# Optimization experiments

Measured on AMD Instinct MI355X. Metric: run time of the kernel, lower is better.

Reference implementation:

```python
import jax, jax.numpy as jnp
import numpy as np

N = 40000      # nodes
E = 320000     # edges (avg degree 8)
F_IN = 128     # input channels
H = 4          # attention heads
C = 64         # per-head hidden channels (hidden_features_size entries)
HC = H * C     # 256, width after head concat
OUT = 64       # output classes
BN_EPS = 1e-5
NEG_SLOPE = 0.2


def setup_inputs() -> dict:
    key = jax.random.key(0)
    ks = jax.random.split(key, 16)
    s1 = 1.0 / np.sqrt(F_IN)
    s2 = 1.0 / np.sqrt(HC)
    return {
        "x": jax.random.normal(ks[0], (N, F_IN), jnp.float32),
        "edge_index": jax.random.randint(ks[1], (2, E), 0, N, dtype=jnp.int64),
        "W1": jax.random.normal(ks[2], (F_IN, HC), jnp.float32) * s1,
        "a1_src": jax.random.normal(ks[3], (H, C), jnp.float32) * s2,
        "a1_dst": jax.random.normal(ks[4], (H, C), jnp.float32) * s2,
        "b1": jnp.zeros((HC,), jnp.float32),
        # BatchNorm1d(256)
        "bn1_gamma": jnp.ones((HC,), jnp.float32),
        "bn1_beta": jnp.zeros((HC,), jnp.float32),
        "W2": jax.random.normal(ks[5], (HC, HC), jnp.float32) * s2,
        "a2_src": jax.random.normal(ks[6], (H, C), jnp.float32) * s2,
        "a2_dst": jax.random.normal(ks[7], (H, C), jnp.float32) * s2,
        "b2": jnp.zeros((HC,), jnp.float32),
        # final projection Linear(256 -> 64)
        "linW": jax.random.normal(ks[8], (HC, OUT), jnp.float32) * s2,
        "linb": jnp.zeros((OUT,), jnp.float32),
    }


def gat_conv(x, W, a_src, a_dst, bias, src, dst):
    """PyG GATConv (concat=True, add_self_loops=False, negative_slope=0.2)."""
    h = (x @ W).reshape(-1, H, C)                       # [N,H,C]
    e_src = jnp.einsum("nhc,hc->nh", h, a_src)          # [N,H]
    e_dst = jnp.einsum("nhc,hc->nh", h, a_dst)          # [N,H]
    # per-edge unnormalized attention, message src -> dst
    e = jax.nn.leaky_relu(e_src[src] + e_dst[dst], NEG_SLOPE)   # [E,H]
    # segment softmax over incoming edges of each dst node
    m = jax.ops.segment_max(e, dst, num_segments=N)             # [N,H]
    p = jnp.exp(e - jax.lax.stop_gradient(m)[dst])              # [E,H]
    denom = jax.ops.segment_sum(p, dst, num_segments=N)         # [N,H]
    alpha = p / (denom[dst] + 1e-16)                            # [E,H]
    # weighted scatter-sum aggregation
    out = jax.ops.segment_sum(h[src] * alpha[:, :, None], dst, num_segments=N)  # [N,H,C]
    return out.reshape(-1, HC) + bias


def batch_norm(x, gamma, beta):
    mean = jnp.mean(x, axis=0)
    var = jnp.mean(jnp.square(x - mean), axis=0)
    return (x - mean) * jax.lax.rsqrt(var + BN_EPS) * gamma + beta


def reference(x, edge_index, W1, a1_src, a1_dst, b1, bn1_gamma, bn1_beta,
              W2, a2_src, a2_dst, b2, linW, linb):
    src, dst = edge_index[0], edge_index[1]
    h1 = gat_conv(x, W1, a1_src, a1_dst, b1, src, dst)
    h1 = jax.nn.elu(batch_norm(h1, bn1_gamma, bn1_beta))
    # dropout is identity in eval mode
    h2 = gat_conv(h1, W2, a2_src, a2_dst, b2, src, dst)
    # JumpingKnowledge 'max': elementwise max over layer outputs
    jk = jnp.maximum(h1, h2)
    return jk @ linW + linb
```

## Files before the change

kernel.cpp:

```cpp
#include <hip/hip_runtime.h>
#include <math.h>

#define N_NODES 40000
#define N_EDGES 320000
#define F_IN 128
#define NHEAD 4
#define HC 256
#define NOUT 64
#define SLOTCAP 40
#define BN_RBLK 40

typedef __attribute__((ext_vector_type(8))) __bf16 bf16x8;
typedef __attribute__((ext_vector_type(4))) float f32x4;

static __device__ __forceinline__ unsigned short f2bf(float f) {
    union { float f; unsigned u; } v; v.f = f;
    unsigned r = v.u + 0x7FFFu + ((v.u >> 16) & 1u);
    return (unsigned short)(r >> 16);
}
static __device__ __forceinline__ float bf2f(unsigned short s) {
    union { unsigned u; float f; } v; v.u = ((unsigned)s) << 16;
    return v.f;
}

__global__ __launch_bounds__(256) void prep_kernel(const float* __restrict__ W1,
                                                   const float* __restrict__ W2,
                                                   const float* __restrict__ linW,
                                                   unsigned short* __restrict__ W1t,
                                                   unsigned short* __restrict__ W2t,
                                                   unsigned short* __restrict__ linWt,
                                                   int* __restrict__ zero_ints,
                                                   float* __restrict__ bnacc) {
    int b = blockIdx.x, tid = threadIdx.x;
    if (b < 128) {
        int t = b * 256 + tid;
        int k = t >> 8, n = t & 255;
        W1t[n * 128 + k] = f2bf(W1[t]);
    } else if (b < 384) {
        int t = (b - 128) * 256 + tid;
        int k = t >> 8, n = t & 255;
        W2t[n * 256 + k] = f2bf(W2[t]);
    } else if (b < 448) {
        int t = (b - 384) * 256 + tid;
        int k = t >> 6, n = t & 63;
        linWt[n * 256 + k] = f2bf(linW[t]);
    } else if (b < 488) {
        int i = (b - 448) * 1024 + tid * 4;
        if (i < 40004) *(int4*)(zero_ints + i) = make_int4(0, 0, 0, 0);
    } else {
        if (tid < 512) bnacc[tid] = 0.f;
    }
}

template <int AMODE, int SCATTER>
__global__ __launch_bounds__(256) void gemm_wide(const void* __restrict__ Aptr,
                                                 const unsigned short* __restrict__ Bt,
                                                 const float* __restrict__ sc,
                                                 unsigned short* __restrict__ Cb,
                                                 const float* __restrict__ asrc,
                                                 const float* __restrict__ adst,
                                                 float* __restrict__ es,
                                                 float* __restrict__ ed,
                                                 int K,
                                                 const int* __restrict__ ei,
                                                 int* __restrict__ cursor,
                                                 unsigned short* __restrict__ esorted) {
    __shared__ unsigned short As[2][64 * 32];
    __shared__ unsigned short Bs[2][256 * 32];
    int tid = threadIdx.x;
    if (SCATTER && blockIdx.x >= N_NODES / 64) {
        int e = (blockIdx.x - N_NODES / 64) * 256 + tid;
        if (e < N_EDGES) {
            int d = ei[N_EDGES + e];
            int s = ei[e];
            int pos = atomicAdd(&cursor[d], 1);
            esorted[d * SLOTCAP + pos] = (unsigned short)s;
        }
        return;
    }
    int row0 = blockIdx.x * 64;
    int w = tid >> 6, lane = tid & 63;
    int quad = lane >> 4, l16 = lane & 15;
    f32x4 acc[4][4];
#pragma unroll
    for (int mi = 0; mi < 4; ++mi)
#pragma unroll
        for (int ni = 0; ni < 4; ++ni) acc[mi][ni] = (f32x4){0.f, 0.f, 0.f, 0.f};

    int srow = tid >> 2, schunk = (tid & 3) * 8;
    int brow = tid >> 1, bchunk = (tid & 1) * 16;

    float4 pa0, pa1;
    int4 pai;
    int4 pb[4];
    if (AMODE == 1) {
        const float* Af = (const float*)Aptr;
        size_t base = (size_t)(row0 + srow) * K + schunk;
        pa0 = *(const float4*)(Af + base);
        pa1 = *(const float4*)(Af + base + 4);
    } else {
        pai = *(const int4*)((const unsigned short*)Aptr + (size_t)(row0 + srow) * K + schunk);
    }
    {
        const unsigned short* s0 = Bt + (size_t)brow * K + bchunk;
        const unsigned short* s1 = Bt + (size_t)(128 + brow) * K + bchunk;
        pb[0] = *(const int4*)s0; pb[1] = *(const int4*)(s0 + 8);
        pb[2] = *(const int4*)s1; pb[3] = *(const int4*)(s1 + 8);
    }

    for (int kc = 0; kc < K; kc += 32) {
        int buf = (kc >> 5) & 1;
        union { int4 v; unsigned short u[8]; } aS;
        if (AMODE == 1) {
            aS.u[0] = f2bf(pa0.x); aS.u[1] = f2bf(pa0.y);
            aS.u[2] = f2bf(pa0.z); aS.u[3] = f2bf(pa0.w);
            aS.u[4] = f2bf(pa1.x); aS.u[5] = f2bf(pa1.y);
            aS.u[6] = f2bf(pa1.z); aS.u[7] = f2bf(pa1.w);
        } else {
            union { int4 v; unsigned short u[8]; } a;
            a.v = pai;
#pragma unroll
            for (int j = 0; j < 8; ++j) {
                int c = kc + schunk + j;
                float v = bf2f(a.u[j]) * sc[c] + sc[HC + c];
                v = v > 0.f ? v : (__expf(v) - 1.f);
                aS.u[j] = f2bf(v);
            }
        }
        int4 bS0 = pb[0], bS1 = pb[1], bS2 = pb[2], bS3 = pb[3];
        int kn = kc + 32;
        if (kn < K) {
            if (AMODE == 1) {
                const float* Af = (const float*)Aptr;
                size_t base = (size_t)(row0 + srow) * K + kn + schunk;
                pa0 = *(const float4*)(Af + base);
                pa1 = *(const float4*)(Af + base + 4);
            } else {
                pai = *(const int4*)((const unsigned short*)Aptr +
                                     (size_t)(row0 + srow) * K + kn + schunk);
            }
            const unsigned short* s0 = Bt + (size_t)brow * K + kn + bchunk;
            const unsigned short* s1 = Bt + (size_t)(128 + brow) * K + kn + bchunk;
            pb[0] = *(const int4*)s0; pb[1] = *(const int4*)(s0 + 8);
            pb[2] = *(const int4*)s1; pb[3] = *(const int4*)(s1 + 8);
        }
        *(int4*)(&As[buf][srow * 32 + schunk]) = aS.v;
        *(int4*)(&Bs[buf][brow * 32 + bchunk]) = bS0;
        *(int4*)(&Bs[buf][brow * 32 + bchunk + 8]) = bS1;
        *(int4*)(&Bs[buf][(128 + brow) * 32 + bchunk]) = bS2;
        *(int4*)(&Bs[buf][(128 + brow) * 32 + bchunk + 8]) = bS3;
        __syncthreads();
        bf16x8 af[4], bfr[4];
#pragma unroll
        for (int mi = 0; mi < 4; ++mi)
            af[mi] = *(const bf16x8*)(&As[buf][(mi * 16 + l16) * 32 + quad * 8]);
#pragma unroll
        for (int ni = 0; ni < 4; ++ni)
            bfr[ni] = *(const bf16x8*)(&Bs[buf][(w * 64 + ni * 16 + l16) * 32 + quad * 8]);
#pragma unroll
        for (int mi = 0; mi < 4; ++mi)
#pragma unroll
            for (int ni = 0; ni < 4; ++ni)
                acc[mi][ni] = __builtin_amdgcn_mfma_f32_16x16x32_bf16(
                    af[mi], bfr[ni], acc[mi][ni], 0, 0, 0);
    }
#pragma unroll
    for (int mi = 0; mi < 4; ++mi)
#pragma unroll
        for (int ni = 0; ni < 4; ++ni) {
            int r0 = row0 + mi * 16 + quad * 4;
            int c = w * 64 + ni * 16 + l16;
#pragma unroll
            for (int r = 0; r < 4; ++r)
                Cb[(size_t)(r0 + r) * HC + c] = f2bf(acc[mi][ni][r]);
        }
    float as_v[4], ad_v[4];
#pragma unroll
    for (int ni = 0; ni < 4; ++ni) {
        int cl = ni * 16 + l16;
        as_v[ni] = asrc[w * 64 + cl];
        ad_v[ni] = adst[w * 64 + cl];
    }
#pragma unroll
    for (int mi = 0; mi < 4; ++mi)
#pragma unroll
        for (int r = 0; r < 4; ++r) {
            float s = 0.f, d = 0.f;
#pragma unroll
            for (int ni = 0; ni < 4; ++ni) {
                s += acc[mi][ni][r] * as_v[ni];
                d += acc[mi][ni][r] * ad_v[ni];
            }
#pragma unroll
            for (int off = 1; off < 16; off <<= 1) {
                s += __shfl_xor(s, off);
                d += __shfl_xor(d, off);
            }
            if (l16 == 0) {
                int row = row0 + mi * 16 + quad * 4 + r;
                es[(size_t)row * NHEAD + w] = s;
                ed[(size_t)row * NHEAD + w] = d;
            }
        }
}

__global__ __launch_bounds__(256) void aggregate_kernel(const unsigned short* __restrict__ h,
                                                        const float* __restrict__ es,
                                                        const float* __restrict__ ed,
                                                        const int* __restrict__ deg,
                                                        const unsigned short* __restrict__ esorted,
                                                        const float* __restrict__ bias,
                                                        unsigned short* __restrict__ outb,
                                                        float* __restrict__ partials) {
    __shared__ float sdata[8][256];
    int tid = threadIdx.x;
    int wave = tid >> 6, lane = tid & 63;
    int half = lane >> 5, l = lane & 31;
    int nloc = wave * 2 + half;
    int node = blockIdx.x * 8 + nloc;
    int hh = l >> 3;
    float edv = ed[node * NHEAD + hh];
    int d = deg[node];
    int beg = node * SLOTCAP;
    float dsum = 0.f;
    float a[8] = {0.f, 0.f, 0.f, 0.f, 0.f, 0.f, 0.f, 0.f};
    for (int i = 0; i < d; i += 16) {
        int s[16];
        int4 hv[16];
        float ep[16];
#pragma unroll
        for (int j = 0; j < 16; ++j) {
            int slot = i + j;
            s[j] = esorted[beg + (slot < d ? slot : d - 1)];
        }
#pragma unroll
        for (int j = 0; j < 16; ++j)
            hv[j] = *(const int4*)(h + (size_t)s[j] * HC + l * 8);
#pragma unroll
        for (int j = 0; j < 16; ++j)
            ep[j] = es[s[j] * NHEAD + hh];
#pragma unroll
        for (int j = 0; j < 16; ++j) {
            float e = ep[j] + edv;
            e = e > 0.f ? e : 0.2f * e;
            float w = __expf(e);
            w = (i + j < d) ? w : 0.f;
            dsum += w;
            union { int4 v; unsigned short u[8]; } hu;
            hu.v = hv[j];
#pragma unroll
            for (int k = 0; k < 8; ++k) a[k] += w * bf2f(hu.u[k]);
        }
    }
    float inv = 1.f / (dsum + 1e-16f);
    float4 bv0 = *(const float4*)(bias + l * 8);
    float4 bv1 = *(const float4*)(bias + l * 8 + 4);
    float bb[8] = {bv0.x, bv0.y, bv0.z, bv0.w, bv1.x, bv1.y, bv1.z, bv1.w};
    float ov[8];
    union { int4 v; unsigned short u[8]; } o;
#pragma unroll
    for (int k = 0; k < 8; ++k) {
        ov[k] = a[k] * inv + bb[k];
        o.u[k] = f2bf(ov[k]);
    }
    *(int4*)(outb + (size_t)node * HC + l * 8) = o.v;
#pragma unroll
    for (int k = 0; k < 8; ++k) sdata[nloc][l * 8 + k] = ov[k];
    __syncthreads();
    {
        int c = tid;
        float s = 0.f, s2 = 0.f;
#pragma unroll
        for (int n = 0; n < 8; ++n) {
            float v = sdata[n][c];
            s += v; s2 += v * v;
        }
        float* pb = partials + (size_t)blockIdx.x * 512;
        pb[c] = s;
        pb[256 + c] = s2;
    }
}

__global__ __launch_bounds__(512) void aggregate2_fused(const unsigned short* __restrict__ h,
                                                        const float* __restrict__ es,
                                                        const float* __restrict__ ed,
                                                        const int* __restrict__ deg,
                                                        const unsigned short* __restrict__ esorted,
                                                        const float* __restrict__ bias,
                                                        const unsigned short* __restrict__ h1agg,
                                                        const float* __restrict__ bnsc,
                                                        const unsigned short* __restrict__ linWt,
                                                        const float* __restrict__ linb,
                                                        float* __restrict__ out) {
    __shared__ unsigned short jkS[16 * 264];
    __shared__ unsigned short BsF[64 * 264];
    int tid = threadIdx.x;
    {
        int n = tid >> 3, k0 = (tid & 7) * 32;
        const int4* src = (const int4*)(linWt + n * 256 + k0);
        int4 v0 = src[0], v1 = src[1], v2 = src[2], v3 = src[3];
        int4* dstp = (int4*)(&BsF[n * 264 + k0]);
        dstp[0] = v0; dstp[1] = v1; dstp[2] = v2; dstp[3] = v3;
    }
    int wave = tid >> 6, lane = tid & 63;
    int half = lane >> 5, l = lane & 31;
    int nloc = wave * 2 + half;
    int node = blockIdx.x * 16 + nloc;
    int hh = l >> 3;
    float edv = ed[node * NHEAD + hh];
    int d = deg[node];
    int beg = node * SLOTCAP;
    float dsum = 0.f;
    float a[8] = {0.f, 0.f, 0.f, 0.f, 0.f, 0.f, 0.f, 0.f};
    for (int i = 0; i < d; i += 8) {
        int s[8];
        int4 hv[8];
        float ep[8];
#pragma unroll
        for (int j = 0; j < 8; ++j) {
            int slot = i + j;
            s[j] = esorted[beg + (slot < d ? slot : d - 1)];
        }
#pragma unroll
        for (int j = 0; j < 8; ++j)
            hv[j] = *(const int4*)(h + (size_t)s[j] * HC + l * 8);
#pragma unroll
        for (int j = 0; j < 8; ++j)
            ep[j] = es[s[j] * NHEAD + hh];
#pragma unroll
        for (int j = 0; j < 8; ++j) {
            float e = ep[j] + edv;
            e = e > 0.f ? e : 0.2f * e;
            float w = __expf(e);
            w = (i + j < d) ? w : 0.f;
            dsum += w;
            union { int4 v; unsigned short u[8]; } hu;
            hu.v = hv[j];
#pragma unroll
            for (int k = 0; k < 8; ++k) a[k] += w * bf2f(hu.u[k]);
        }
    }
    float inv = 1.f / (dsum + 1e-16f);
    float4 bv0 = *(const float4*)(bias + l * 8);
    float4 bv1 = *(const float4*)(bias + l * 8 + 4);
    float bb[8] = {bv0.x, bv0.y, bv0.z, bv0.w, bv1.x, bv1.y, bv1.z, bv1.w};
    union { int4 v; unsigned short u[8]; } o;
    {
        union { int4 v; unsigned short u[8]; } h1u;
        h1u.v = *(const int4*)(h1agg + (size_t)node * HC + l * 8);
        float4 s0 = *(const float4*)(bnsc + l * 8);
        float4 s1 = *(const float4*)(bnsc + l * 8 + 4);
        float4 t0 = *(const float4*)(bnsc + HC + l * 8);
        float4 t1 = *(const float4*)(bnsc + HC + l * 8 + 4);
        float scv[8] = {s0.x, s0.y, s0.z, s0.w, s1.x, s1.y, s1.z, s1.w};
        float shv[8] = {t0.x, t0.y, t0.z, t0.w, t1.x, t1.y, t1.z, t1.w};
#pragma unroll
        for (int k = 0; k < 8; ++k) {
            float v = bf2f(h1u.u[k]) * scv[k] + shv[k];
            v = v > 0.f ? v : (__expf(v) - 1.f);
            o.u[k] = f2bf(fmaxf(v, a[k] * inv + bb[k]));
        }
    }
    *(int4*)(&jkS[nloc * 264 + l * 8]) = o.v;
    __syncthreads();
    if (wave < 4) {
        int quad = lane >> 4, l16 = lane & 15;
        f32x4 acc = (f32x4){0.f, 0.f, 0.f, 0.f};
#pragma unroll
        for (int kc = 0; kc < HC; kc += 32) {
            bf16x8 af = *(const bf16x8*)(&jkS[l16 * 264 + kc + quad * 8]);
            bf16x8 bfr = *(const bf16x8*)(&BsF[(wave * 16 + l16) * 264 + kc + quad * 8]);
            acc = __builtin_amdgcn_mfma_f32_16x16x32_bf16(af, bfr, acc, 0, 0, 0);
        }
        int row0 = blockIdx.x * 16 + quad * 4;
        int c = wave * 16 + l16;
        float bc = linb[c];
#pragma unroll
        for (int r = 0; r < 4; ++r)
            out[(size_t)(row0 + r) * NOUT + c] = acc[r] + bc;
    }
}

__global__ __launch_bounds__(256) void bn_reduce_kernel(const float* __restrict__ partials,
                                                        float* __restrict__ acc,
                                                        const float* __restrict__ gamma,
                                                        const float* __restrict__ beta,
                                                        float* __restrict__ sc,
                                                        int* __restrict__ ticket) {
    int t = threadIdx.x;
    const int per = (N_NODES / 8) / BN_RBLK;
    int b0 = blockIdx.x * per;
    float A = 0.f, B = 0.f;
    for (int b = b0; b < b0 + per; ++b) {
        A += partials[(size_t)b * 512 + t];
        B += partials[(size_t)b * 512 + 256 + t];
    }
    atomicAdd(&acc[t], A);
    atomicAdd(&acc[HC + t], B);
    __threadfence();
    __syncthreads();
    __shared__ int is_last;
    if (t == 0) is_last = (atomicAdd(ticket, 1) == BN_RBLK - 1);
    __syncthreads();
    if (is_last) {
        float sum = atomicAdd(&acc[t], 0.f);
        float sq  = atomicAdd(&acc[HC + t], 0.f);
        float mean = sum * (1.f / N_NODES);
        float var = sq * (1.f / N_NODES) - mean * mean;
        float inv = rsqrtf(var + 1e-5f);
        float scale = gamma[t] * inv;
        sc[t] = scale;
        sc[HC + t] = beta[t] - mean * scale;
    }
}

extern "C" void kernel_launch(void* const* d_in, const int* in_sizes, int n_in,
                              void* d_out, int out_size, void* d_ws, size_t ws_size,
                              hipStream_t stream) {
    const float* x      = (const float*)d_in[0];
    const int*   ei     = (const int*)d_in[1];
    const float* W1     = (const float*)d_in[2];
    const float* a1_src = (const float*)d_in[3];
    const float* a1_dst = (const float*)d_in[4];
    const float* b1     = (const float*)d_in[5];
    const float* bn_g   = (const float*)d_in[6];
    const float* bn_b   = (const float*)d_in[7];
    const float* W2     = (const float*)d_in[8];
    const float* a2_src = (const float*)d_in[9];
    const float* a2_dst = (const float*)d_in[10];
    const float* b2     = (const float*)d_in[11];
    const float* linW   = (const float*)d_in[12];
    const float* linb   = (const float*)d_in[13];
    float* out = (float*)d_out;

    char* ws = (char*)d_ws;
    const size_t NHC_BF = (size_t)N_NODES * HC * 2;
    unsigned short* hpre_b  = (unsigned short*)(ws);
    unsigned short* h1agg_b = (unsigned short*)(ws + NHC_BF);
    float* partials = (float*)(ws + 2 * NHC_BF);
    char* p = ws + 4 * NHC_BF;
    unsigned short* W1t   = (unsigned short*)p; p += (size_t)F_IN * HC * 2;
    unsigned short* W2t   = (unsigned short*)p; p += (size_t)HC * HC * 2;
    unsigned short* linWt = (unsigned short*)p; p += (size_t)HC * NOUT * 2;
    float* e_src   = (float*)p;  p += (size_t)N_NODES * NHEAD * 4;
    float* e_dst   = (float*)p;  p += (size_t)N_NODES * NHEAD * 4;
    int*   cursor  = (int*)p;    p += (size_t)N_NODES * 4;
    int*   ticket  = (int*)p;    p += 4 * 4;
    unsigned short* esorted = (unsigned short*)p; p += (size_t)N_NODES * SLOTCAP * 2;
    float* bnacc   = (float*)p;  p += 2 * HC * 4;
    float* bnsc    = (float*)p;  p += 2 * HC * 4;

    prep_kernel<<<489, 256, 0, stream>>>(W1, W2, linW, W1t, W2t, linWt, cursor, bnacc);

    gemm_wide<1, 1><<<N_NODES / 64 + (N_EDGES + 255) / 256, 256, 0, stream>>>(
        x, W1t, nullptr, hpre_b, a1_src, a1_dst, e_src, e_dst, F_IN,
        ei, cursor, esorted);

    aggregate_kernel<<<N_NODES / 8, 256, 0, stream>>>(
        hpre_b, e_src, e_dst, cursor, esorted, b1, h1agg_b, partials);

    bn_reduce_kernel<<<BN_RBLK, 256, 0, stream>>>(partials, bnacc, bn_g, bn_b,
                                                  bnsc, ticket);

    gemm_wide<3, 0><<<N_NODES / 64, 256, 0, stream>>>(
        h1agg_b, W2t, bnsc, hpre_b, a2_src, a2_dst, e_src, e_dst, HC,
        nullptr, nullptr, nullptr);

    aggregate2_fused<<<N_NODES / 16, 512, 0, stream>>>(
        hpre_b, e_src, e_dst, cursor, esorted, b2, h1agg_b, bnsc, linWt, linb, out);
}
```

Measured before the change: 220.4 us.

## Sort nodes by in-degree to balance aggregation work across waves

Adds a histogram and placement pass that builds a permutation of nodes grouped by in-degree, then both aggregation kernels process nodes in that order and write outputs through the permutation. The goal is to reduce divergence and tail imbalance, since nodes sharing a wave or block now have similar edge counts. It costs two extra small kernel launches, scattered output writes, and less spatial locality in node-indexed reads.

```diff
diff --git a/kernel.cpp b/kernel.cpp
--- a/kernel.cpp
+++ b/kernel.cpp
@@ -9,6 +9,7 @@
 #define NOUT 64
 #define SLOTCAP 40
 #define BN_RBLK 40
+#define NBIN 44
 
 typedef __attribute__((ext_vector_type(8))) __bf16 bf16x8;
 typedef __attribute__((ext_vector_type(4))) float f32x4;
@@ -46,7 +47,7 @@
         linWt[n * 256 + k] = f2bf(linW[t]);
     } else if (b < 488) {
         int i = (b - 448) * 1024 + tid * 4;
-        if (i < 40004) *(int4*)(zero_ints + i) = make_int4(0, 0, 0, 0);
+        if (i < 40092) *(int4*)(zero_ints + i) = make_int4(0, 0, 0, 0);
     } else {
         if (tid < 512) bnacc[tid] = 0.f;
     }
@@ -204,11 +205,58 @@
         }
 }
 
+__global__ __launch_bounds__(256) void sort_hist_kernel(const int* __restrict__ deg,
+                                                        int* __restrict__ bins,
+                                                        int* __restrict__ ticket) {
+    int n = blockIdx.x * 256 + threadIdx.x;
+    if (n < N_NODES) {
+        int d = deg[n];
+        if (d > NBIN - 1) d = NBIN - 1;
+        atomicAdd(&bins[d], 1);
+    }
+    __threadfence();
+    __syncthreads();
+    __shared__ int is_last;
+    if (threadIdx.x == 0) is_last = (atomicAdd(&ticket[1], 1) == (int)gridDim.x - 1);
+    __syncthreads();
+    if (is_last && threadIdx.x == 0) {
+        int run = 0;
+        for (int d = 0; d < NBIN; ++d) {
+            int t = atomicAdd(&bins[d], 0);
+            bins[d] = run;
+            run += t;
+        }
+    }
+}
+
+__global__ __launch_bounds__(256) void place_kernel(const int* __restrict__ deg,
+                                                    const int* __restrict__ bins,
+                                                    int* __restrict__ cnt,
+                                                    unsigned short* __restrict__ perm) {
+    __shared__ int lcnt[NBIN], lbase[NBIN];
+    int tid = threadIdx.x;
+    if (tid < NBIN) lcnt[tid] = 0;
+    __syncthreads();
+    int n = blockIdx.x * 256 + tid;
+    int d = 0, r = 0;
+    bool act = n < N_NODES;
+    if (act) {
+        d = deg[n];
+        if (d > NBIN - 1) d = NBIN - 1;
+        r = atomicAdd(&lcnt[d], 1);
+    }
+    __syncthreads();
+    if (tid < NBIN) lbase[tid] = lcnt[tid] ? atomicAdd(&cnt[tid], lcnt[tid]) : 0;
+    __syncthreads();
+    if (act) perm[bins[d] + lbase[d] + r] = (unsigned short)n;
+}
+
 __global__ __launch_bounds__(256) void aggregate_kernel(const unsigned short* __restrict__ h,
                                                         const float* __restrict__ es,
                                                         const float* __restrict__ ed,
                                                         const int* __restrict__ deg,
                                                         const unsigned short* __restrict__ esorted,
+                                                        const unsigned short* __restrict__ perm,
                                                         const float* __restrict__ bias,
                                                         unsigned short* __restrict__ outb,
                                                         float* __restrict__ partials) {
@@ -217,7 +265,7 @@
     int wave = tid >> 6, lane = tid & 63;
     int half = lane >> 5, l = lane & 31;
     int nloc = wave * 2 + half;
-    int node = blockIdx.x * 8 + nloc;
+    int node = perm[blockIdx.x * 8 + nloc];
     int hh = l >> 3;
     float edv = ed[node * NHEAD + hh];
     int d = deg[node];
@@ -286,6 +334,7 @@
                                                         const float* __restrict__ ed,
                                                         const int* __restrict__ deg,
                                                         const unsigned short* __restrict__ esorted,
+                                                        const unsigned short* __restrict__ perm,
                                                         const float* __restrict__ bias,
                                                         const unsigned short* __restrict__ h1agg,
                                                         const float* __restrict__ bnsc,
@@ -294,6 +343,7 @@
                                                         float* __restrict__ out) {
     __shared__ unsigned short jkS[16 * 264];
     __shared__ unsigned short BsF[64 * 264];
+    __shared__ int nodeS[16];
     int tid = threadIdx.x;
     {
         int n = tid >> 3, k0 = (tid & 7) * 32;
@@ -305,7 +355,8 @@
     int wave = tid >> 6, lane = tid & 63;
     int half = lane >> 5, l = lane & 31;
     int nloc = wave * 2 + half;
-    int node = blockIdx.x * 16 + nloc;
+    int node = perm[blockIdx.x * 16 + nloc];
+    if ((lane & 31) == 0) nodeS[nloc] = node;
     int hh = l >> 3;
     float edv = ed[node * NHEAD + hh];
     int d = deg[node];
@@ -372,12 +423,13 @@
             bf16x8 bfr = *(const bf16x8*)(&BsF[(wave * 16 + l16) * 264 + kc + quad * 8]);
             acc = __builtin_amdgcn_mfma_f32_16x16x32_bf16(af, bfr, acc, 0, 0, 0);
         }
-        int row0 = blockIdx.x * 16 + quad * 4;
         int c = wave * 16 + l16;
         float bc = linb[c];
 #pragma unroll
-        for (int r = 0; r < 4; ++r)
-            out[(size_t)(row0 + r) * NOUT + c] = acc[r] + bc;
+        for (int r = 0; r < 4; ++r) {
+            int m = quad * 4 + r;
+            out[(size_t)nodeS[m] * NOUT + c] = acc[r] + bc;
+        }
     }
 }
 
@@ -446,7 +498,10 @@
     float* e_dst   = (float*)p;  p += (size_t)N_NODES * NHEAD * 4;
     int*   cursor  = (int*)p;    p += (size_t)N_NODES * 4;
     int*   ticket  = (int*)p;    p += 4 * 4;
+    int*   bins    = (int*)p;    p += NBIN * 4;
+    int*   cnt     = (int*)p;    p += NBIN * 4;
     unsigned short* esorted = (unsigned short*)p; p += (size_t)N_NODES * SLOTCAP * 2;
+    unsigned short* perm    = (unsigned short*)p; p += (size_t)N_NODES * 2;
     float* bnacc   = (float*)p;  p += 2 * HC * 4;
     float* bnsc    = (float*)p;  p += 2 * HC * 4;
 
@@ -456,8 +511,11 @@
         x, W1t, nullptr, hpre_b, a1_src, a1_dst, e_src, e_dst, F_IN,
         ei, cursor, esorted);
 
+    sort_hist_kernel<<<(N_NODES + 255) / 256, 256, 0, stream>>>(cursor, bins, ticket);
+    place_kernel<<<(N_NODES + 255) / 256, 256, 0, stream>>>(cursor, bins, cnt, perm);
+
     aggregate_kernel<<<N_NODES / 8, 256, 0, stream>>>(
-        hpre_b, e_src, e_dst, cursor, esorted, b1, h1agg_b, partials);
+        hpre_b, e_src, e_dst, cursor, esorted, perm, b1, h1agg_b, partials);
 
     bn_reduce_kernel<<<BN_RBLK, 256, 0, stream>>>(partials, bnacc, bn_g, bn_b,
                                                   bnsc, ticket);
@@ -467,5 +525,6 @@
         nullptr, nullptr, nullptr);
 
     aggregate2_fused<<<N_NODES / 16, 512, 0, stream>>>(
-        hpre_b, e_src, e_dst, cursor, esorted, b2, h1agg_b, bnsc, linWt, linb, out);
-}
+        hpre_b, e_src, e_dst, cursor, esorted, perm, b2, h1agg_b, bnsc,
+        linWt, linb, out);
+}
```

After: 376.2 us. 1.71x slower.
